# Kernel tuning notes

Hardware: AMD Instinct MI355X
Metric: run time of the kernel (lower is better)

The kernel has to match this reference:

```python
import jax, jax.numpy as jnp
import numpy as np

D_MODEL = 256
NHEAD = 8
NLAYERS = 4
DFF = 1024
PATCH = 8
INPUT = 32
C = 2
DATA_DIM = C * PATCH * PATCH  # 128
P = (INPUT // PATCH) ** 2     # 16
NEG = -1.0e6                  # _neg_large_for_dtype(float32)
EPS = 1e-5


def _ln(x, w, b):
    m = x.mean(-1, keepdims=True)
    v = ((x - m) ** 2).mean(-1, keepdims=True)
    return (x - m) / jnp.sqrt(v + EPS) * w + b


def _forward(img_baseline, acq_dts_float, nan_token, pad_embed, emb_w, emb_b, spatial_pos,
             t_w1, t_b1, t_w2, t_b2, t_w3, t_b3,
             in_proj_w, in_proj_b, out_proj_w, out_proj_b,
             lin1_w, lin1_b, lin2_w, lin2_b, norm1_w, norm1_b, norm2_w, norm2_b,
             mean_w1, mean_b1, mean_w2, mean_b2, lv_w1, lv_b1, lv_w2, lv_b2):
    B, T, Cc, Hh, Ww = img_baseline.shape
    p = PATCH
    gh, gw = Hh // p, Ww // p
    L = T * P
    frame_pad = jnp.all(img_baseline == -9999.0, axis=(2, 3, 4))  # (B,T)
    nan_pix = jnp.isnan(img_baseline)
    token = jnp.clip(nan_token, -10.0, 10.0).reshape(1, 1, Cc, 1, 1)
    x = jnp.clip(jnp.where(nan_pix, token, img_baseline), -10.0, 10.0)

    def patchify(a):  # b t c (h ph)(w pw) -> b t (h w) (c ph pw)
        return a.reshape(B, T, Cc, gh, p, gw, p).transpose(0, 1, 3, 5, 2, 4, 6).reshape(B, T, P, Cc * p * p)

    xp = patchify(x)
    seq_nan = patchify(nan_pix).all(-1).reshape(B, L)
    seq_pad = jnp.broadcast_to(frame_pad[:, :, None], (B, T, P)).reshape(B, L)

    # temporal MLP embedding
    t_in = jnp.where(jnp.isnan(acq_dts_float), 0.0, acq_dts_float)[..., None]  # (B,T,1)
    h = jax.nn.relu(t_in @ t_w1.T + t_b1)
    h = jax.nn.relu(h @ t_w2.T + t_b2)
    temb = h @ t_w3.T + t_b3  # (B,T,D)

    z = xp @ emb_w.T + emb_b + spatial_pos + temb[:, :, None, :]  # (B,T,P,D)
    z = z.reshape(B, L, D_MODEL)
    z = jnp.where(seq_pad[..., None], pad_embed, z)  # masked_scatter of pad_embed

    # additive attention mask: rows with NaN/pad patches are fully masked except diagonal
    masked_rows = seq_nan | seq_pad
    mask = jnp.broadcast_to(jnp.where(masked_rows[:, :, None], NEG, 0.0), (B, L, L))
    eye = jnp.eye(L, dtype=bool)
    mask = jnp.where(eye[None, :, :] & masked_rows[:, :, None], 0.0, mask)
    # key_padding_mask merged additively on key columns
    mask = mask + jnp.where(seq_pad[:, None, :], NEG, 0.0)
    mask = mask[:, None, :, :]  # (B,1,L,L), shared across heads

    dh = D_MODEL // NHEAD
    scale = 1.0 / np.sqrt(dh).astype(np.float32)
    for l in range(NLAYERS):
        qkv = z @ in_proj_w[l].T + in_proj_b[l]
        q, k, v = jnp.split(qkv, 3, axis=-1)
        q = q.reshape(B, L, NHEAD, dh).transpose(0, 2, 1, 3)
        k = k.reshape(B, L, NHEAD, dh).transpose(0, 2, 1, 3)
        v = v.reshape(B, L, NHEAD, dh).transpose(0, 2, 1, 3)
        scores = jnp.einsum('bhqd,bhkd->bhqk', q, k) * scale + mask
        attn = jax.nn.softmax(scores, axis=-1)
        o = jnp.einsum('bhqk,bhkd->bhqd', attn, v).transpose(0, 2, 1, 3).reshape(B, L, D_MODEL)
        o = o @ out_proj_w[l].T + out_proj_b[l]
        z = _ln(z + o, norm1_w[l], norm1_b[l])
        ff = jax.nn.relu(z @ lin1_w[l].T + lin1_b[l]) @ lin2_w[l].T + lin2_b[l]
        z = _ln(z + ff, norm2_w[l], norm2_b[l])

    mean = jnp.clip(jax.nn.relu(z @ mean_w1.T + mean_b1) @ mean_w2.T + mean_b2, -10.0, 10.0)
    logvar = jnp.clip(jax.nn.relu(z @ lv_w1.T + lv_b1) @ lv_w2.T + lv_b2, -10.0, 5.0)

    def unpatch(a):  # b t (h w)(c ph pw) -> b t c (h ph)(w pw)
        return a.reshape(B, T, gh, gw, Cc, p, p).transpose(0, 1, 4, 2, 5, 3, 6).reshape(B, T, Cc, Hh, Ww)

    mean = unpatch(mean.reshape(B, T, P, DATA_DIM))
    logvar = unpatch(logvar.reshape(B, T, P, DATA_DIM))
    return mean[:, -1], logvar[:, -1]


def setup_inputs() -> dict:
    key = jax.random.key(0)
    ks = iter(jax.random.split(key, 48))

    def rn(shape, scale=0.02):
        return jax.random.normal(next(ks), shape, dtype=jnp.float32) * scale

    B, T = 4, 64
    z = lambda s: jnp.zeros(s, jnp.float32)
    return {
        'img_baseline': jax.random.normal(next(ks), (B, T, C, INPUT, INPUT), dtype=jnp.float32),
        'acq_dts_float': jax.random.uniform(next(ks), (B, T), dtype=jnp.float32) * 3000.0,
        'nan_token': rn((C,)),
        'pad_embed': rn((1, 1, D_MODEL)),
        'emb_w': rn((D_MODEL, DATA_DIM)),
        'emb_b': z((D_MODEL,)),
        'spatial_pos': rn((1, 1, P, D_MODEL)),
        't_w1': rn((64, 1)), 't_b1': z((64,)),
        't_w2': rn((128, 64)), 't_b2': z((128,)),
        't_w3': rn((D_MODEL, 128)), 't_b3': z((D_MODEL,)),
        'in_proj_w': rn((NLAYERS, 3 * D_MODEL, D_MODEL)),
        'in_proj_b': z((NLAYERS, 3 * D_MODEL)),
        'out_proj_w': rn((NLAYERS, D_MODEL, D_MODEL)),
        'out_proj_b': z((NLAYERS, D_MODEL)),
        'lin1_w': rn((NLAYERS, DFF, D_MODEL)), 'lin1_b': z((NLAYERS, DFF)),
        'lin2_w': rn((NLAYERS, D_MODEL, DFF)), 'lin2_b': z((NLAYERS, D_MODEL)),
        'norm1_w': jnp.ones((NLAYERS, D_MODEL), jnp.float32), 'norm1_b': z((NLAYERS, D_MODEL)),
        'norm2_w': jnp.ones((NLAYERS, D_MODEL), jnp.float32), 'norm2_b': z((NLAYERS, D_MODEL)),
        'mean_w1': rn((DFF, D_MODEL)), 'mean_b1': z((DFF,)),
        'mean_w2': rn((DATA_DIM, DFF)), 'mean_b2': z((DATA_DIM,)),
        'lv_w1': rn((DFF, D_MODEL)), 'lv_b1': z((DFF,)),
        'lv_w2': rn((DATA_DIM, DFF)), 'lv_b2': z((DATA_DIM,)),
    }


def reference(img_baseline, acq_dts_float, nan_token, pad_embed, emb_w, emb_b, spatial_pos,
              t_w1, t_b1, t_w2, t_b2, t_w3, t_b3,
              in_proj_w, in_proj_b, out_proj_w, out_proj_b,
              lin1_w, lin1_b, lin2_w, lin2_b, norm1_w, norm1_b, norm2_w, norm2_b,
              mean_w1, mean_b1, mean_w2, mean_b2, lv_w1, lv_b1, lv_w2, lv_b2):
    return _forward(img_baseline, acq_dts_float, nan_token, pad_embed, emb_w, emb_b, spatial_pos,
                    t_w1, t_b1, t_w2, t_b2, t_w3, t_b3,
                    in_proj_w, in_proj_b, out_proj_w, out_proj_b,
                    lin1_w, lin1_b, lin2_w, lin2_b, norm1_w, norm1_b, norm2_w, norm2_b,
                    mean_w1, mean_b1, mean_w2, mean_b2, lv_w1, lv_b1, lv_w2, lv_b2)
```

## Files before the change

kernel.cpp:

```cpp
#include <hip/hip_runtime.h>
#include <hip/hip_bf16.h>

#define D_MODEL 256
#define NHEAD 8
#define DH 32
#define NLAYERS 4
#define DFF 1024
#define CC 2
#define DATA_DIM 128
#define PP 16
#define TT 64
#define BB 4
#define LL 1024
#define NEGV -1000000.0f

typedef __bf16 bf16_t;
typedef __bf16 bf16x8 __attribute__((ext_vector_type(8)));
typedef __bf16 bf16x4 __attribute__((ext_vector_type(4)));
typedef float v4f __attribute__((ext_vector_type(4)));

__device__ __forceinline__ bool my_isnan(float v) {
    unsigned u = __float_as_uint(v);
    return (u & 0x7fffffffu) > 0x7f800000u;
}

__device__ __forceinline__ void gld16(bf16_t* l, const bf16_t* g) {
    __builtin_amdgcn_global_load_lds(
        (const __attribute__((address_space(1))) void*)g,
        (__attribute__((address_space(3))) void*)l, 16, 0, 0);
}

__global__ __launch_bounds__(256) void f2b_prep_kernel(
    const float* __restrict__ in_proj_w, bf16_t* __restrict__ inb,
    const float* __restrict__ out_proj_w, bf16_t* __restrict__ outb,
    const float* __restrict__ lin1_w, bf16_t* __restrict__ l1b,
    const float* __restrict__ lin2_w, bf16_t* __restrict__ l2b,
    const float* __restrict__ emb_w, bf16_t* __restrict__ embwb,
    const float* __restrict__ mean_w1, const float* __restrict__ lv_w1, bf16_t* __restrict__ w1b,
    const float* __restrict__ mean_w2, const float* __restrict__ lv_w2, bf16_t* __restrict__ w2b,
    const float* __restrict__ img, const float* __restrict__ acq,
    const float* __restrict__ t_w1, const float* __restrict__ t_b1,
    const float* __restrict__ t_w2, const float* __restrict__ t_b2,
    const float* __restrict__ t_w3, const float* __restrict__ t_b3,
    float* __restrict__ temb, int* __restrict__ framepad) {
    const int n0 = NLAYERS * 768 * D_MODEL;
    const int n1 = NLAYERS * D_MODEL * D_MODEL;
    const int n2 = NLAYERS * DFF * D_MODEL;
    const int n3 = NLAYERS * D_MODEL * DFF;
    const int n4 = D_MODEL * DATA_DIM;
    const int n5 = DFF * D_MODEL;
    const int n6 = DFF * D_MODEL;
    const int n7 = DATA_DIM * DFF;
    const int n8 = DATA_DIM * DFF;
    int tid = threadIdx.x;
    int i = (blockIdx.x * 256 + tid) * 4;
    const float* s = nullptr; bf16_t* d = nullptr;
    if (i < n0) { s = in_proj_w; d = inb; }
    else if ((i -= n0) < n1) { s = out_proj_w; d = outb; }
    else if ((i -= n1) < n2) { s = lin1_w; d = l1b; }
    else if ((i -= n2) < n3) { s = lin2_w; d = l2b; }
    else if ((i -= n3) < n4) { s = emb_w; d = embwb; }
    else if ((i -= n4) < n5) { s = mean_w1; d = w1b; }
    else if ((i -= n5) < n6) { s = lv_w1; d = w1b + n5; }
    else if ((i -= n6) < n7) { s = mean_w2; d = w2b; }
    else if ((i -= n7) < n8) { s = lv_w2; d = w2b + n7; }
    if (s) {
        float4 v = *(const float4*)(s + i);
        bf16x4 o = {(bf16_t)v.x, (bf16_t)v.y, (bf16_t)v.z, (bf16_t)v.w};
        *(bf16x4*)(d + i) = o;
    }

    if (blockIdx.x >= BB * TT) return;
    int f = blockIdx.x;
    __shared__ float h1[64];
    __shared__ float h2[128];
    __shared__ int sAll;
    if (tid == 0) sAll = 1;
    __syncthreads();
    const float* fr = img + (size_t)f * (CC * 32 * 32);
    bool allpad = true;
    #pragma unroll
    for (int k = 0; k < 8; ++k) {
        float v = fr[tid + k * 256];
        allpad = allpad && (v == -9999.0f);
    }
    if (!allpad) sAll = 0;
    __syncthreads();
    if (tid == 0) framepad[f] = sAll;

    float t_in = acq[f];
    if (my_isnan(t_in)) t_in = 0.0f;
    if (tid < 64) h1[tid] = fmaxf(t_w1[tid] * t_in + t_b1[tid], 0.0f);
    __syncthreads();
    if (tid < 128) {
        float a = t_b2[tid];
        #pragma unroll 8
        for (int j = 0; j < 64; ++j) a += t_w2[tid * 64 + j] * h1[j];
        h2[tid] = fmaxf(a, 0.0f);
    }
    __syncthreads();
    {
        float a = t_b3[tid];
        #pragma unroll 8
        for (int j = 0; j < 128; ++j) a += t_w3[tid * 128 + j] * h2[j];
        temb[(size_t)f * D_MODEL + tid] = a;
    }
}

__global__ __launch_bounds__(256) void patchify_kernel(
    const float* __restrict__ img, const float* __restrict__ nan_token,
    const int* __restrict__ framepad,
    bf16_t* __restrict__ xpb, int* __restrict__ masked_rows,
    float* __restrict__ kmaskf) {
    int tid = threadIdx.x;
    int token = blockIdx.x * 2 + (tid >> 7);
    int dd = tid & 127;
    int l = token & 1023, b = token >> 10;
    int t = l >> 4, p = l & 15;
    int c = dd >> 6, pr = (dd >> 3) & 7, pc = dd & 7;
    int hh = (p >> 2) * 8 + pr, ww = (p & 3) * 8 + pc;
    float v = img[(((size_t)(b * TT + t) * CC + c) * 32 + hh) * 32 + ww];
    bool nanp = my_isnan(v);
    if (nanp) v = fminf(fmaxf(nan_token[c], -10.0f), 10.0f);
    v = fminf(fmaxf(v, -10.0f), 10.0f);
    xpb[(size_t)token * DATA_DIM + dd] = (bf16_t)v;

    __shared__ int wAll[4];
    unsigned long long bal = __ballot(nanp);
    if ((tid & 63) == 0) wAll[tid >> 6] = (bal == 0xFFFFFFFFFFFFFFFFull) ? 1 : 0;
    __syncthreads();
    if (tid < 2) {
        int tk = blockIdx.x * 2 + tid;
        int allnan = wAll[tid * 2] & wAll[tid * 2 + 1];
        int fp = framepad[tk >> 4];
        masked_rows[tk] = allnan | fp;
        kmaskf[tk] = fp ? NEGV : 0.0f;
    }
}

__global__ __launch_bounds__(256) void embed_gemm(
    const bf16_t* __restrict__ X, const bf16_t* __restrict__ W,
    const float* __restrict__ emb_b, const float* __restrict__ spatial,
    const float* __restrict__ temb, const float* __restrict__ pad_embed,
    const int* __restrict__ framepad,
    bf16_t* __restrict__ zb) {
    __shared__ __align__(16) bf16_t Xs[2][128 * 64];
    __shared__ __align__(16) bf16_t Ws[2][64 * 64];
    int tid = threadIdx.x;
    int wave = tid >> 6, lane = tid & 63;
    int quad = lane >> 4, l16 = lane & 15;
    int m0 = blockIdx.y * 128, n0 = blockIdx.x * 64;
    const int K = DATA_DIM, N = D_MODEL;

    v4f acc[2][4];
    #pragma unroll
    for (int i = 0; i < 2; ++i)
        #pragma unroll
        for (int j = 0; j < 4; ++j) acc[i][j] = (v4f){0.f, 0.f, 0.f, 0.f};

    int sr = tid >> 3, ss = tid & 7;
    int gc = (ss ^ (sr & 7)) * 8;

#define ESTAGE(bufi, k0)                                                          \
    do {                                                                          \
        _Pragma("unroll")                                                         \
        for (int p = 0; p < 4; ++p) {                                             \
            int r = sr + p * 32;                                                  \
            gld16(Xs[bufi] + r * 64 + ss * 8, X + (size_t)(m0 + r) * K + (k0) + gc); \
        }                                                                         \
        _Pragma("unroll")                                                         \
        for (int p = 0; p < 2; ++p) {                                             \
            int r = sr + p * 32;                                                  \
            gld16(Ws[bufi] + r * 64 + ss * 8, W + (size_t)(n0 + r) * K + (k0) + gc); \
        }                                                                         \
    } while (0)

    ESTAGE(0, 0);
    __syncthreads();
    const int T = K / 64;
    int swl = l16 & 7;
    for (int t = 0; t < T; ++t) {
        int buf = t & 1;
        if (t + 1 < T) ESTAGE(buf ^ 1, (t + 1) * 64);
        const bf16_t* Xc = Xs[buf];
        const bf16_t* Wc = Ws[buf];
        int ra = wave * 32 + l16;
        #pragma unroll
        for (int h = 0; h < 2; ++h) {
            int g8 = ((h * 4 + quad) ^ swl) * 8;
            bf16x8 af0 = *(const bf16x8*)(Xc + ra * 64 + g8);
            bf16x8 af1 = *(const bf16x8*)(Xc + (ra + 16) * 64 + g8);
            #pragma unroll
            for (int nt = 0; nt < 4; ++nt) {
                bf16x8 bfr = *(const bf16x8*)(Wc + (nt * 16 + l16) * 64 + g8);
                acc[0][nt] = __builtin_amdgcn_mfma_f32_16x16x32_bf16(af0, bfr, acc[0][nt], 0, 0, 0);
                acc[1][nt] = __builtin_amdgcn_mfma_f32_16x16x32_bf16(af1, bfr, acc[1][nt], 0, 0, 0);
            }
        }
        __syncthreads();
    }
#undef ESTAGE

    #pragma unroll
    for (int mt = 0; mt < 2; ++mt)
        #pragma unroll
        for (int nt = 0; nt < 4; ++nt) {
            int col = n0 + nt * 16 + l16;
            #pragma unroll
            for (int reg = 0; reg < 4; ++reg) {
                int row = m0 + wave * 32 + mt * 16 + quad * 4 + reg;
                int frame = row >> 4, p = row & 15;
                float v;
                if (framepad[frame]) {
                    v = pad_embed[col];
                } else {
                    v = acc[mt][nt][reg] + emb_b[col] + spatial[p * N + col]
                      + temb[(size_t)frame * N + col];
                }
                zb[(size_t)row * N + col] = (bf16_t)v;
            }
        }
}

template <int MODE, int RELU>
__global__ __launch_bounds__(256) void gemm_mfma(
    const bf16_t* __restrict__ X, const bf16_t* __restrict__ W,
    const float* __restrict__ bias, bf16_t* __restrict__ Y,
    bf16_t* __restrict__ Vt, int M, int N, int K) {
    __shared__ __align__(16) bf16_t Xs[3][128 * 64];
    __shared__ __align__(16) bf16_t Ws[3][64 * 64];
    int tid = threadIdx.x;
    int wave = tid >> 6, lane = tid & 63;
    int quad = lane >> 4, l16 = lane & 15;
    int m0 = blockIdx.y * 128, n0 = blockIdx.x * 64;

    v4f acc[2][4];
    #pragma unroll
    for (int i = 0; i < 2; ++i)
        #pragma unroll
        for (int j = 0; j < 4; ++j) acc[i][j] = (v4f){0.f, 0.f, 0.f, 0.f};

    int sr = tid >> 3, ss = tid & 7;
    int gc = (ss ^ (sr & 7)) * 8;

#define GSTAGE(bufi, k0)                                                          \
    do {                                                                          \
        _Pragma("unroll")                                                         \
        for (int p = 0; p < 4; ++p) {                                             \
            int r = sr + p * 32;                                                  \
            gld16(Xs[bufi] + r * 64 + ss * 8, X + (size_t)(m0 + r) * K + (k0) + gc); \
        }                                                                         \
        _Pragma("unroll")                                                         \
        for (int p = 0; p < 2; ++p) {                                             \
            int r = sr + p * 32;                                                  \
            gld16(Ws[bufi] + r * 64 + ss * 8, W + (size_t)(n0 + r) * K + (k0) + gc); \
        }                                                                         \
    } while (0)

    const int T = K >> 6;
    GSTAGE(0, 0);
    if (T > 1) GSTAGE(1, 64);
    int swl = l16 & 7;
    for (int t = 0; t < T; ++t) {
        int buf = t % 3;
        if (t + 1 < T) asm volatile("s_waitcnt vmcnt(6)" ::: "memory");
        else           asm volatile("s_waitcnt vmcnt(0)" ::: "memory");
        __builtin_amdgcn_s_barrier();
        __builtin_amdgcn_sched_barrier(0);
        if (t + 2 < T) GSTAGE((t + 2) % 3, (t + 2) * 64);
        const bf16_t* Xc = Xs[buf];
        const bf16_t* Wc = Ws[buf];
        int ra = wave * 32 + l16;
        #pragma unroll
        for (int h = 0; h < 2; ++h) {
            int g8 = ((h * 4 + quad) ^ swl) * 8;
            bf16x8 af0 = *(const bf16x8*)(Xc + ra * 64 + g8);
            bf16x8 af1 = *(const bf16x8*)(Xc + (ra + 16) * 64 + g8);
            #pragma unroll
            for (int nt = 0; nt < 4; ++nt) {
                bf16x8 bfr = *(const bf16x8*)(Wc + (nt * 16 + l16) * 64 + g8);
                acc[0][nt] = __builtin_amdgcn_mfma_f32_16x16x32_bf16(af0, bfr, acc[0][nt], 0, 0, 0);
                acc[1][nt] = __builtin_amdgcn_mfma_f32_16x16x32_bf16(af1, bfr, acc[1][nt], 0, 0, 0);
            }
        }
    }
#undef GSTAGE
    __syncthreads();

    if constexpr (MODE == 1) {
        #pragma unroll
        for (int mt = 0; mt < 2; ++mt)
            #pragma unroll
            for (int nt = 0; nt < 4; ++nt) {
                int col = n0 + nt * 16 + l16;
                float bv = bias[col];
                #pragma unroll
                for (int reg = 0; reg < 4; ++reg) {
                    int row = m0 + wave * 32 + mt * 16 + quad * 4 + reg;
                    float v = acc[mt][nt][reg] + bv;
                    if (RELU) v = fmaxf(v, 0.0f);
                    Y[(size_t)row * N + col] = (bf16_t)v;
                }
            }
    } else {
        if (n0 < 512) {
            #pragma unroll
            for (int mt = 0; mt < 2; ++mt)
                #pragma unroll
                for (int nt = 0; nt < 4; ++nt) {
                    int col = n0 + nt * 16 + l16;
                    float bv = bias[col];
                    #pragma unroll
                    for (int reg = 0; reg < 4; ++reg) {
                        int row = m0 + wave * 32 + mt * 16 + quad * 4 + reg;
                        float v = acc[mt][nt][reg] + bv;
                        Y[(size_t)row * 768 + col] = (bf16_t)v;
                    }
                }
        } else {
            bf16_t* VT = &Xs[0][0];
            #pragma unroll
            for (int mt = 0; mt < 2; ++mt)
                #pragma unroll
                for (int nt = 0; nt < 4; ++nt) {
                    int cl = nt * 16 + l16;
                    float bv = bias[n0 + cl];
                    #pragma unroll
                    for (int reg = 0; reg < 4; ++reg) {
                        int rl = wave * 32 + mt * 16 + quad * 4 + reg;
                        VT[cl * 136 + rl] = (bf16_t)(acc[mt][nt][reg] + bv);
                    }
                }
            __syncthreads();
            int b = m0 >> 10, l0m = m0 & 1023;
            int cl = tid >> 2;
            int rbase = (tid & 3) * 8;
            int cg2 = n0 + cl - 512;
            int h = cg2 >> 5, d = cg2 & 31;
            bf16_t* dst = Vt + (((size_t)(b * NHEAD + h)) * DH + d) * LL + l0m;
            #pragma unroll
            for (int u = 0; u < 4; ++u)
                *(uint4*)(dst + rbase + u * 32) = *(const uint4*)(VT + cl * 136 + rbase + u * 32);
        }
    }
}

__global__ __launch_bounds__(256) void gemm_row_ln(
    const bf16_t* __restrict__ X, const bf16_t* __restrict__ W,
    const float* __restrict__ bias, const bf16_t* __restrict__ Zres,
    bf16_t* __restrict__ Y, const float* __restrict__ lnw,
    const float* __restrict__ lnb, int K) {
    __shared__ __align__(16) bf16_t Xs[3][16 * 64];
    __shared__ __align__(16) bf16_t Ws[3][256 * 64];
    int tid = threadIdx.x;
    int wave = tid >> 6, lane = tid & 63;
    int quad = lane >> 4, l16 = lane & 15;
    int mrow0 = blockIdx.x * 16;

    v4f acc[4];
    #pragma unroll
    for (int j = 0; j < 4; ++j) acc[j] = (v4f){0.f, 0.f, 0.f, 0.f};

    int sr = tid >> 3, ss = tid & 7;
    int gc = (ss ^ (sr & 7)) * 8;
    int xl = lane & 31;
    int xrow = wave * 4 + (xl >> 3);
    int xgc = ((xl & 7) ^ (xrow & 7)) * 8;

#define RSTAGE(bufi, k0)                                                          \
    do {                                                                          \
        if (lane < 32)                                                            \
            gld16(Xs[bufi] + wave * 256 + xl * 8,                                 \
                  X + (size_t)(mrow0 + xrow) * K + (k0) + xgc);                   \
        _Pragma("unroll")                                                         \
        for (int p = 0; p < 8; ++p) {                                             \
            int r = sr + p * 32;                                                  \
            gld16(Ws[bufi] + r * 64 + ss * 8, W + (size_t)r * K + (k0) + gc);     \
        }                                                                         \
    } while (0)

    const int T = K >> 6;
    RSTAGE(0, 0);
    RSTAGE(1, 64);
    int swl = l16 & 7;
    for (int t = 0; t < T; ++t) {
        int buf = t % 3;
        if (t + 1 < T) asm volatile("s_waitcnt vmcnt(9)" ::: "memory");
        else           asm volatile("s_waitcnt vmcnt(0)" ::: "memory");
        __builtin_amdgcn_s_barrier();
        __builtin_amdgcn_sched_barrier(0);
        if (t + 2 < T) RSTAGE((t + 2) % 3, (t + 2) * 64);
        const bf16_t* Xc = Xs[buf];
        const bf16_t* Wc = Ws[buf];
        #pragma unroll
        for (int h = 0; h < 2; ++h) {
            int g8 = ((h * 4 + quad) ^ swl) * 8;
            bf16x8 af = *(const bf16x8*)(Xc + l16 * 64 + g8);
            #pragma unroll
            for (int ntl = 0; ntl < 4; ++ntl) {
                int nt = wave * 4 + ntl;
                bf16x8 bfr = *(const bf16x8*)(Wc + (nt * 16 + l16) * 64 + g8);
                acc[ntl] = __builtin_amdgcn_mfma_f32_16x16x32_bf16(af, bfr, acc[ntl], 0, 0, 0);
            }
        }
    }
#undef RSTAGE
    __syncthreads();

    float* psum = (float*)&Xs[0][0];
    float xv[4][4];
    float lw[4], lb[4];
    #pragma unroll
    for (int ntl = 0; ntl < 4; ++ntl) {
        int col = wave * 64 + ntl * 16 + l16;
        float bv = bias[col];
        lw[ntl] = lnw[col];
        lb[ntl] = lnb[col];
        #pragma unroll
        for (int reg = 0; reg < 4; ++reg) {
            int grow = mrow0 + quad * 4 + reg;
            xv[ntl][reg] = acc[ntl][reg] + bv + (float)Zres[(size_t)grow * D_MODEL + col];
        }
    }
    float s[4];
    #pragma unroll
    for (int reg = 0; reg < 4; ++reg) {
        s[reg] = xv[0][reg] + xv[1][reg] + xv[2][reg] + xv[3][reg];
        s[reg] += __shfl_xor(s[reg], 1);
        s[reg] += __shfl_xor(s[reg], 2);
        s[reg] += __shfl_xor(s[reg], 4);
        s[reg] += __shfl_xor(s[reg], 8);
    }
    if (l16 == 0) {
        #pragma unroll
        for (int reg = 0; reg < 4; ++reg)
            psum[wave * 16 + quad * 4 + reg] = s[reg];
    }
    __syncthreads();
    float mean[4];
    #pragma unroll
    for (int reg = 0; reg < 4; ++reg) {
        int row = quad * 4 + reg;
        mean[reg] = (psum[row] + psum[16 + row] + psum[32 + row] + psum[48 + row])
                  * (1.0f / D_MODEL);
    }
    __syncthreads();
    float q[4];
    #pragma unroll
    for (int reg = 0; reg < 4; ++reg) {
        float d0 = xv[0][reg] - mean[reg], d1 = xv[1][reg] - mean[reg];
        float d2 = xv[2][reg] - mean[reg], d3 = xv[3][reg] - mean[reg];
        q[reg] = d0 * d0 + d1 * d1 + d2 * d2 + d3 * d3;
        q[reg] += __shfl_xor(q[reg], 1);
        q[reg] += __shfl_xor(q[reg], 2);
        q[reg] += __shfl_xor(q[reg], 4);
        q[reg] += __shfl_xor(q[reg], 8);
    }
    if (l16 == 0) {
        #pragma unroll
        for (int reg = 0; reg < 4; ++reg)
            psum[wave * 16 + quad * 4 + reg] = q[reg];
    }
    __syncthreads();
    #pragma unroll
    for (int reg = 0; reg < 4; ++reg) {
        int row = quad * 4 + reg;
        float var = (psum[row] + psum[16 + row] + psum[32 + row] + psum[48 + row])
                  * (1.0f / D_MODEL);
        float inv = 1.0f / sqrtf(var + 1e-5f);
        int grow = mrow0 + row;
        #pragma unroll
        for (int ntl = 0; ntl < 4; ++ntl) {
            int col = wave * 64 + ntl * 16 + l16;
            Y[(size_t)grow * D_MODEL + col] =
                (bf16_t)((xv[ntl][reg] - mean[reg]) * inv * lw[ntl] + lb[ntl]);
        }
    }
}

__global__ __launch_bounds__(256) void attn_mfma(
    const bf16_t* __restrict__ qkvb, const bf16_t* __restrict__ Vt,
    const int* __restrict__ masked_rows, const float* __restrict__ kmaskf,
    bf16_t* __restrict__ Ob) {
    __shared__ __align__(16) bf16_t Ks[2][128 * 40];
    __shared__ __align__(16) bf16_t Vs[2][32 * 136];
    __shared__ __align__(16) float  Kms[2][128];
    __shared__ __align__(16) bf16_t Ps[4][16 * 136];

    int tid = threadIdx.x;
    int wave = tid >> 6, lane = tid & 63;
    int quad = lane >> 4, l16 = lane & 15;
    int bid = blockIdx.x;
    int h = bid & 7, b = (bid >> 3) & 3, qt = bid >> 5;
    int q0 = qt * 64 + wave * 16;
    const float scale = 0.17677669529663687f;

    bf16x8 qf = *(const bf16x8*)(qkvb + ((size_t)(b * LL) + q0 + l16) * 768 + h * DH + quad * 8);

    int mq = masked_rows[b * LL + q0 + l16];
    int qg = q0 + l16;

    float lrun = 0.0f;
    v4f oacc[2];
    oacc[0] = (v4f){0.f, 0.f, 0.f, 0.f};
    oacc[1] = (v4f){0.f, 0.f, 0.f, 0.f};

    int kr = tid >> 1, kh = (tid & 1) * 16;
    int vd = tid >> 3, vs0 = (tid & 7) * 8;
    const bf16_t* Kbase = qkvb + (size_t)(b * LL) * 768 + 256 + h * DH;
    const bf16_t* Vbase = Vt + (((size_t)(b * NHEAD + h)) * DH) * LL;
    const float* kmbase = kmaskf + b * LL;

    uint4 ka, kb, va, vb;
    float kmg;
    #define LOADC(c)                                                            \
        do {                                                                    \
            int _k0 = (c) * 128;                                                \
            ka = *(const uint4*)(Kbase + (size_t)(_k0 + kr) * 768 + kh);        \
            kb = *(const uint4*)(Kbase + (size_t)(_k0 + kr) * 768 + kh + 8);    \
            va = *(const uint4*)(Vbase + (size_t)vd * LL + _k0 + vs0);          \
            vb = *(const uint4*)(Vbase + (size_t)vd * LL + _k0 + 64 + vs0);     \
            kmg = (tid < 128) ? kmbase[_k0 + tid] : 0.0f;                       \
        } while (0)
    #define WRITEBUF(buf)                                                       \
        do {                                                                    \
            *(uint4*)(Ks[(buf)] + kr * 40 + kh) = ka;                           \
            *(uint4*)(Ks[(buf)] + kr * 40 + kh + 8) = kb;                       \
            *(uint4*)(Vs[(buf)] + vd * 136 + vs0) = va;                         \
            *(uint4*)(Vs[(buf)] + vd * 136 + 64 + vs0) = vb;                    \
            if (tid < 128) Kms[(buf)][tid] = kmg;                               \
        } while (0)

    LOADC(0);
    WRITEBUF(0);
    LOADC(1);

    bf16_t* Pw = Ps[wave];
    for (int c = 0; c < 8; ++c) {
        __syncthreads();
        int cur = c & 1;
        if (c + 1 < 8) WRITEBUF(cur ^ 1);
        if (c + 2 < 8) LOADC(c + 2);

        int k0 = c * 128;
        const bf16_t* Kc = Ks[cur];
        const bf16_t* Vc = Vs[cur];
        const float* kmc = Kms[cur];

        v4f sf[8];
        #pragma unroll
        for (int nt = 0; nt < 8; ++nt) {
            bf16x8 kf = *(const bf16x8*)(Kc + (nt * 16 + l16) * 40 + quad * 8);
            v4f zf = (v4f){0.f, 0.f, 0.f, 0.f};
            sf[nt] = __builtin_amdgcn_mfma_f32_16x16x32_bf16(kf, qf, zf, 0, 0, 0);
        }

        #pragma unroll
        for (int nt = 0; nt < 8; ++nt) {
            int kbase_nt = k0 + nt * 16 + quad * 4;
            float4 kmv = *(const float4*)(kmc + nt * 16 + quad * 4);
            float pv[4];
            #pragma unroll
            for (int reg = 0; reg < 4; ++reg) {
                float km = (reg == 0) ? kmv.x : (reg == 1) ? kmv.y : (reg == 2) ? kmv.z : kmv.w;
                float v = sf[nt][reg] * scale + km;
                if (mq && (qg != kbase_nt + reg)) v += NEGV;
                float p = __expf(v);
                lrun += p;
                pv[reg] = p;
            }
            bf16x4 pp = {(bf16_t)pv[0], (bf16_t)pv[1], (bf16_t)pv[2], (bf16_t)pv[3]};
            *(bf16x4*)(Pw + l16 * 136 + nt * 16 + quad * 4) = pp;
        }

        #pragma unroll
        for (int kt = 0; kt < 4; ++kt) {
            bf16x8 pf = *(const bf16x8*)(Pw + l16 * 136 + kt * 32 + quad * 8);
            #pragma unroll
            for (int nt2 = 0; nt2 < 2; ++nt2) {
                bf16x8 vf = *(const bf16x8*)(Vc + (nt2 * 16 + l16) * 136 + kt * 32 + quad * 8);
                oacc[nt2] = __builtin_amdgcn_mfma_f32_16x16x32_bf16(pf, vf, oacc[nt2], 0, 0, 0);
            }
        }
    }
    #undef LOADC
    #undef WRITEBUF

    lrun += __shfl_xor(lrun, 16);
    lrun += __shfl_xor(lrun, 32);
    float lq[4];
    #pragma unroll
    for (int reg = 0; reg < 4; ++reg) lq[reg] = __shfl(lrun, quad * 4 + reg);

    #pragma unroll
    for (int nt2 = 0; nt2 < 2; ++nt2)
        #pragma unroll
        for (int reg = 0; reg < 4; ++reg) {
            size_t row = (size_t)(b * LL) + q0 + quad * 4 + reg;
            Ob[row * 256 + h * DH + nt2 * 16 + l16] = (bf16_t)(oacc[nt2][reg] / lq[reg]);
        }
}

__global__ __launch_bounds__(256) void head_h_kernel(
    const bf16_t* __restrict__ zb, const bf16_t* __restrict__ W1b,
    const float* __restrict__ mean_b1, const float* __restrict__ lv_b1,
    bf16_t* __restrict__ hb) {
    __shared__ __align__(16) bf16_t Xs[2][64 * 32 * 2];
    __shared__ __align__(16) bf16_t Ws[2][64 * 32 * 2];
    int tid = threadIdx.x;
    int wave = tid >> 6, lane = tid & 63;
    int quad = lane >> 4, l16 = lane & 15;
    int head = blockIdx.y;
    int n0 = blockIdx.x * 64;
    const bf16_t* W1h = W1b + (size_t)head * DFF * D_MODEL;
    const float* B1f = head ? lv_b1 : mean_b1;
    bf16_t* hbh = hb + (size_t)head * 64 * DFF;

    v4f acc[4];
    #pragma unroll
    for (int j = 0; j < 4; ++j) acc[j] = (v4f){0.f, 0.f, 0.f, 0.f};

    int sr = tid >> 3, ss = tid & 7;
    int gc = (ss ^ (sr & 7)) * 8;

#define HSTAGE(bufi, k0)                                                          \
    do {                                                                          \
        _Pragma("unroll")                                                         \
        for (int p = 0; p < 2; ++p) {                                             \
            int r = sr + p * 32;                                                  \
            const bf16_t* xr = zb + (size_t)((r >> 4) * LL + (TT - 1) * PP + (r & 15)) * D_MODEL; \
            gld16(Xs[bufi] + r * 64 + ss * 8, xr + (k0) + gc);                    \
            gld16(Ws[bufi] + r * 64 + ss * 8, W1h + (size_t)(n0 + r) * D_MODEL + (k0) + gc); \
        }                                                                         \
    } while (0)

    HSTAGE(0, 0);
    __syncthreads();
    const int T = D_MODEL / 64;
    int swl = l16 & 7;
    for (int t = 0; t < T; ++t) {
        int buf = t & 1;
        if (t + 1 < T) HSTAGE(buf ^ 1, (t + 1) * 64);
        const bf16_t* Xc = Xs[buf];
        const bf16_t* Wc = Ws[buf];
        int ra = wave * 16 + l16;
        #pragma unroll
        for (int h = 0; h < 2; ++h) {
            int g8 = ((h * 4 + quad) ^ swl) * 8;
            bf16x8 af = *(const bf16x8*)(Xc + ra * 64 + g8);
            #pragma unroll
            for (int nt = 0; nt < 4; ++nt) {
                bf16x8 bfr = *(const bf16x8*)(Wc + (nt * 16 + l16) * 64 + g8);
                acc[nt] = __builtin_amdgcn_mfma_f32_16x16x32_bf16(af, bfr, acc[nt], 0, 0, 0);
            }
        }
        __syncthreads();
    }
#undef HSTAGE

    #pragma unroll
    for (int nt = 0; nt < 4; ++nt) {
        int col = n0 + nt * 16 + l16;
        float bv = B1f[col];
        #pragma unroll
        for (int reg = 0; reg < 4; ++reg) {
            int row = wave * 16 + quad * 4 + reg;
            hbh[(size_t)row * DFF + col] = (bf16_t)fmaxf(acc[nt][reg] + bv, 0.0f);
        }
    }
}

__global__ __launch_bounds__(256) void head_out_kernel(
    const bf16_t* __restrict__ hb, const bf16_t* __restrict__ W2b,
    const float* __restrict__ mean_b2, const float* __restrict__ lv_b2,
    float* __restrict__ out) {
    __shared__ __align__(16) bf16_t hrow[DFF];
    int tid = threadIdx.x;
    int bid = blockIdx.x;
    int head = bid >> 7, rr = (bid >> 1) & 63, half = bid & 1;
    int b = rr >> 4, p = rr & 15;

    if (tid < 128)
        *(uint4*)(hrow + tid * 8) =
            *(const uint4*)(hb + ((size_t)head * 64 + rr) * DFF + tid * 8);
    __syncthreads();

    int ol = tid >> 2, quarter = tid & 3;
    int o = half * 64 + ol;
    const bf16_t* wrow = W2b + ((size_t)head * DATA_DIM + o) * DFF + quarter * 256;
    const bf16_t* hseg = hrow + quarter * 256;
    float acc = 0.0f;
    #pragma unroll 8
    for (int j = 0; j < 32; ++j) {
        bf16x8 w = *(const bf16x8*)(wrow + j * 8);
        bf16x8 hv = *(const bf16x8*)(hseg + j * 8);
        #pragma unroll
        for (int e = 0; e < 8; ++e) acc += (float)w[e] * (float)hv[e];
    }
    acc += __shfl_xor(acc, 1);
    acc += __shfl_xor(acc, 2);
    if (quarter == 0) {
        const float* B2 = head ? lv_b2 : mean_b2;
        float hi = head ? 5.0f : 10.0f;
        float v = fminf(fmaxf(acc + B2[o], -10.0f), hi);
        int c = o >> 6;
        int pr = (o >> 3) & 7, pc = o & 7;
        int hh = (p >> 2) * 8 + pr, ww = (p & 3) * 8 + pc;
        out[(size_t)head * 8192 + ((size_t)(b * CC + c)) * 1024 + hh * 32 + ww] = v;
    }
}

extern "C" void kernel_launch(void* const* d_in, const int* in_sizes, int n_in,
                              void* d_out, int out_size, void* d_ws, size_t ws_size,
                              hipStream_t stream) {
    const float* img        = (const float*)d_in[0];
    const float* acq        = (const float*)d_in[1];
    const float* nan_token  = (const float*)d_in[2];
    const float* pad_embed  = (const float*)d_in[3];
    const float* emb_w      = (const float*)d_in[4];
    const float* emb_b      = (const float*)d_in[5];
    const float* spatial    = (const float*)d_in[6];
    const float* t_w1       = (const float*)d_in[7];
    const float* t_b1       = (const float*)d_in[8];
    const float* t_w2       = (const float*)d_in[9];
    const float* t_b2       = (const float*)d_in[10];
    const float* t_w3       = (const float*)d_in[11];
    const float* t_b3       = (const float*)d_in[12];
    const float* in_proj_w  = (const float*)d_in[13];
    const float* in_proj_b  = (const float*)d_in[14];
    const float* out_proj_w = (const float*)d_in[15];
    const float* out_proj_b = (const float*)d_in[16];
    const float* lin1_w     = (const float*)d_in[17];
    const float* lin1_b     = (const float*)d_in[18];
    const float* lin2_w     = (const float*)d_in[19];
    const float* lin2_b     = (const float*)d_in[20];
    const float* norm1_w    = (const float*)d_in[21];
    const float* norm1_b    = (const float*)d_in[22];
    const float* norm2_w    = (const float*)d_in[23];
    const float* norm2_b    = (const float*)d_in[24];
    const float* mean_w1    = (const float*)d_in[25];
    const float* mean_b1    = (const float*)d_in[26];
    const float* mean_w2    = (const float*)d_in[27];
    const float* mean_b2    = (const float*)d_in[28];
    const float* lv_w1      = (const float*)d_in[29];
    const float* lv_b1      = (const float*)d_in[30];
    const float* lv_w2      = (const float*)d_in[31];
    const float* lv_b2      = (const float*)d_in[32];

    const int M = BB * LL;

    char* wsb = (char*)d_ws;
    float* temb    = (float*)wsb;                    wsb += (size_t)BB * TT * D_MODEL * 4;
    float* kmaskf  = (float*)wsb;                    wsb += M * 4;
    int* framepad  = (int*)wsb;                      wsb += BB * TT * 4;
    int* masked    = (int*)wsb;                      wsb += M * 4;
    wsb = (char*)(((uintptr_t)wsb + 255) & ~(uintptr_t)255);
    bf16_t* zb     = (bf16_t*)wsb;                   wsb += (size_t)M * D_MODEL * 2;
    bf16_t* xpb    = (bf16_t*)wsb;                   wsb += (size_t)M * DATA_DIM * 2;
    bf16_t* qkvb   = (bf16_t*)wsb;                   wsb += (size_t)M * 768 * 2;
    bf16_t* VtG    = (bf16_t*)wsb;                   wsb += (size_t)M * D_MODEL * 2;
    bf16_t* attnb  = (bf16_t*)wsb;                   wsb += (size_t)M * D_MODEL * 2;
    bf16_t* ff1b   = (bf16_t*)wsb;                   wsb += (size_t)M * DFF * 2;
    bf16_t* inb    = (bf16_t*)wsb;                   wsb += (size_t)NLAYERS * 768 * D_MODEL * 2;
    bf16_t* outb   = (bf16_t*)wsb;                   wsb += (size_t)NLAYERS * D_MODEL * D_MODEL * 2;
    bf16_t* l1b    = (bf16_t*)wsb;                   wsb += (size_t)NLAYERS * DFF * D_MODEL * 2;
    bf16_t* l2b    = (bf16_t*)wsb;                   wsb += (size_t)NLAYERS * D_MODEL * DFF * 2;
    bf16_t* embwb  = (bf16_t*)wsb;                   wsb += (size_t)D_MODEL * DATA_DIM * 2;
    bf16_t* w1b    = (bf16_t*)wsb;                   wsb += (size_t)2 * DFF * D_MODEL * 2;
    bf16_t* w2b    = (bf16_t*)wsb;                   wsb += (size_t)2 * DATA_DIM * DFF * 2;
    bf16_t* hb     = (bf16_t*)wsb;                   wsb += (size_t)2 * 64 * DFF * 2;

    float* outF = (float*)d_out;

    {
        int tot = NLAYERS * 768 * D_MODEL + NLAYERS * D_MODEL * D_MODEL +
                  NLAYERS * DFF * D_MODEL + NLAYERS * D_MODEL * DFF +
                  D_MODEL * DATA_DIM + 2 * DFF * D_MODEL + 2 * DATA_DIM * DFF;
        f2b_prep_kernel<<<(tot / 4 + 255) / 256, 256, 0, stream>>>(
            in_proj_w, inb, out_proj_w, outb, lin1_w, l1b, lin2_w, l2b,
            emb_w, embwb, mean_w1, lv_w1, w1b, mean_w2, lv_w2, w2b,
            img, acq, t_w1, t_b1, t_w2, t_b2, t_w3, t_b3, temb, framepad);
    }

    patchify_kernel<<<M / 2, 256, 0, stream>>>(img, nan_token, framepad, xpb, masked, kmaskf);
    embed_gemm<<<dim3(D_MODEL / 64, M / 128), 256, 0, stream>>>(
        xpb, embwb, emb_b, spatial, temb, pad_embed, framepad, zb);

    for (int l = 0; l < NLAYERS; ++l) {
        gemm_mfma<2, 0><<<dim3(768 / 64, M / 128), 256, 0, stream>>>(
            zb, inb + (size_t)l * 768 * D_MODEL, in_proj_b + (size_t)l * 768,
            qkvb, VtG, M, 768, D_MODEL);
        attn_mfma<<<BB * NHEAD * (LL / 64), 256, 0, stream>>>(qkvb, VtG, masked, kmaskf, attnb);
        gemm_row_ln<<<M / 16, 256, 0, stream>>>(
            attnb, outb + (size_t)l * D_MODEL * D_MODEL, out_proj_b + (size_t)l * D_MODEL,
            zb, zb, norm1_w + l * D_MODEL, norm1_b + l * D_MODEL, D_MODEL);
        gemm_mfma<1, 1><<<dim3(DFF / 64, M / 128), 256, 0, stream>>>(
            zb, l1b + (size_t)l * DFF * D_MODEL, lin1_b + (size_t)l * DFF,
            ff1b, nullptr, M, DFF, D_MODEL);
        gemm_row_ln<<<M / 16, 256, 0, stream>>>(
            ff1b, l2b + (size_t)l * D_MODEL * DFF, lin2_b + (size_t)l * D_MODEL,
            zb, zb, norm2_w + l * D_MODEL, norm2_b + l * D_MODEL, DFF);
    }

    head_h_kernel<<<dim3(DFF / 64, 2), 256, 0, stream>>>(zb, w1b, mean_b1, lv_b1, hb);
    head_out_kernel<<<256, 256, 0, stream>>>(hb, w2b, mean_b2, lv_b2, outF);
}
```

Baseline: 389.8 us.

## Fuse out-proj+LayerNorm with FF1 GEMM+ReLU in one row-block kernel

```diff
diff --git a/kernel.cpp b/kernel.cpp
--- a/kernel.cpp
+++ b/kernel.cpp
@@ -478,6 +478,204 @@
     }
 }
 
+__global__ __launch_bounds__(256) void gemm_row_ln_ff(
+    const bf16_t* __restrict__ X, const bf16_t* __restrict__ W,
+    const float* __restrict__ bias, const bf16_t* __restrict__ Zres,
+    bf16_t* __restrict__ Y, const float* __restrict__ lnw,
+    const float* __restrict__ lnb,
+    const bf16_t* __restrict__ W1, const float* __restrict__ b1,
+    bf16_t* __restrict__ H) {
+    __shared__ __align__(16) bf16_t Xs[3][16 * 64];
+    __shared__ __align__(16) bf16_t Ynorm[16 * 256];
+    __shared__ __align__(16) bf16_t Ws[3][256 * 64];
+    int tid = threadIdx.x;
+    int wave = tid >> 6, lane = tid & 63;
+    int quad = lane >> 4, l16 = lane & 15;
+    int mrow0 = blockIdx.x * 16;
+    const int K = D_MODEL;
+
+    v4f acc[4];
+    #pragma unroll
+    for (int j = 0; j < 4; ++j) acc[j] = (v4f){0.f, 0.f, 0.f, 0.f};
+
+    int sr = tid >> 3, ss = tid & 7;
+    int gc = (ss ^ (sr & 7)) * 8;
+    int xl = lane & 31;
+    int xrow = wave * 4 + (xl >> 3);
+    int xgc = ((xl & 7) ^ (xrow & 7)) * 8;
+    int swl = l16 & 7;
+
+#define ASTAGE(bufi, k0)                                                          \
+    do {                                                                          \
+        if (lane < 32)                                                            \
+            gld16(Xs[bufi] + wave * 256 + xl * 8,                                 \
+                  X + (size_t)(mrow0 + xrow) * K + (k0) + xgc);                   \
+        _Pragma("unroll")                                                         \
+        for (int p = 0; p < 8; ++p) {                                             \
+            int r = sr + p * 32;                                                  \
+            gld16(Ws[bufi] + r * 64 + ss * 8, W + (size_t)r * K + (k0) + gc);     \
+        }                                                                         \
+    } while (0)
+
+    const int TA = K >> 6;
+    ASTAGE(0, 0);
+    ASTAGE(1, 64);
+    for (int t = 0; t < TA; ++t) {
+        int buf = t % 3;
+        if (t + 1 < TA) asm volatile("s_waitcnt vmcnt(9)" ::: "memory");
+        else            asm volatile("s_waitcnt vmcnt(0)" ::: "memory");
+        __builtin_amdgcn_s_barrier();
+        __builtin_amdgcn_sched_barrier(0);
+        if (t + 2 < TA) ASTAGE((t + 2) % 3, (t + 2) * 64);
+        const bf16_t* Xc = Xs[buf];
+        const bf16_t* Wc = Ws[buf];
+        #pragma unroll
+        for (int h = 0; h < 2; ++h) {
+            int g8 = ((h * 4 + quad) ^ swl) * 8;
+            bf16x8 af = *(const bf16x8*)(Xc + l16 * 64 + g8);
+            #pragma unroll
+            for (int ntl = 0; ntl < 4; ++ntl) {
+                int nt = wave * 4 + ntl;
+                bf16x8 bfr = *(const bf16x8*)(Wc + (nt * 16 + l16) * 64 + g8);
+                acc[ntl] = __builtin_amdgcn_mfma_f32_16x16x32_bf16(af, bfr, acc[ntl], 0, 0, 0);
+            }
+        }
+    }
+#undef ASTAGE
+    __syncthreads();
+
+#define BSTAGE(bufi, s)                                                           \
+    do {                                                                          \
+        int _pn = (s) >> 2, _ks = (s) & 3;                                        \
+        _Pragma("unroll")                                                         \
+        for (int p = 0; p < 8; ++p) {                                             \
+            int r = sr + p * 32;                                                  \
+            gld16(Ws[bufi] + r * 64 + ss * 8,                                     \
+                  W1 + (size_t)(_pn * 256 + r) * 256 + _ks * 64 + gc);            \
+        }                                                                         \
+    } while (0)
+
+    BSTAGE(0, 0);
+    BSTAGE(1, 1);
+
+    float* psum = (float*)&Xs[0][0];
+    float xv[4][4];
+    float lw[4], lb[4];
+    #pragma unroll
+    for (int ntl = 0; ntl < 4; ++ntl) {
+        int col = wave * 64 + ntl * 16 + l16;
+        float bv = bias[col];
+        lw[ntl] = lnw[col];
+        lb[ntl] = lnb[col];
+        #pragma unroll
+        for (int reg = 0; reg < 4; ++reg) {
+            int grow = mrow0 + quad * 4 + reg;
+            xv[ntl][reg] = acc[ntl][reg] + bv + (float)Zres[(size_t)grow * D_MODEL + col];
+        }
+    }
+    float s1[4];
+    #pragma unroll
+    for (int reg = 0; reg < 4; ++reg) {
+        s1[reg] = xv[0][reg] + xv[1][reg] + xv[2][reg] + xv[3][reg];
+        s1[reg] += __shfl_xor(s1[reg], 1);
+        s1[reg] += __shfl_xor(s1[reg], 2);
+        s1[reg] += __shfl_xor(s1[reg], 4);
+        s1[reg] += __shfl_xor(s1[reg], 8);
+    }
+    if (l16 == 0) {
+        #pragma unroll
+        for (int reg = 0; reg < 4; ++reg)
+            psum[wave * 16 + quad * 4 + reg] = s1[reg];
+    }
+    __syncthreads();
+    float mean[4];
+    #pragma unroll
+    for (int reg = 0; reg < 4; ++reg) {
+        int row = quad * 4 + reg;
+        mean[reg] = (psum[row] + psum[16 + row] + psum[32 + row] + psum[48 + row])
+                  * (1.0f / D_MODEL);
+    }
+    __syncthreads();
+    float q[4];
+    #pragma unroll
+    for (int reg = 0; reg < 4; ++reg) {
+        float d0 = xv[0][reg] - mean[reg], d1 = xv[1][reg] - mean[reg];
+        float d2 = xv[2][reg] - mean[reg], d3 = xv[3][reg] - mean[reg];
+        q[reg] = d0 * d0 + d1 * d1 + d2 * d2 + d3 * d3;
+        q[reg] += __shfl_xor(q[reg], 1);
+        q[reg] += __shfl_xor(q[reg], 2);
+        q[reg] += __shfl_xor(q[reg], 4);
+        q[reg] += __shfl_xor(q[reg], 8);
+    }
+    if (l16 == 0) {
+        #pragma unroll
+        for (int reg = 0; reg < 4; ++reg)
+            psum[wave * 16 + quad * 4 + reg] = q[reg];
+    }
+    __syncthreads();
+    #pragma unroll
+    for (int reg = 0; reg < 4; ++reg) {
+        int row = quad * 4 + reg;
+        float var = (psum[row] + psum[16 + row] + psum[32 + row] + psum[48 + row])
+                  * (1.0f / D_MODEL);
+        float inv = 1.0f / sqrtf(var + 1e-5f);
+        int grow = mrow0 + row;
+        #pragma unroll
+        for (int ntl = 0; ntl < 4; ++ntl) {
+            int col = wave * 64 + ntl * 16 + l16;
+            float nv = (xv[ntl][reg] - mean[reg]) * inv * lw[ntl] + lb[ntl];
+            bf16_t nb = (bf16_t)nv;
+            Y[(size_t)grow * D_MODEL + col] = nb;
+            int within = ntl * 16 + l16;
+            int g = within >> 3;
+            int slot = g ^ (row & 7);
+            Ynorm[row * 256 + wave * 64 + slot * 8 + (within & 7)] = nb;
+        }
+    }
+    __syncthreads();
+
+    v4f accB[4];
+    #pragma unroll
+    for (int j = 0; j < 4; ++j) accB[j] = (v4f){0.f, 0.f, 0.f, 0.f};
+
+    for (int s = 0; s < 16; ++s) {
+        int buf = s % 3;
+        if (s + 1 < 16) asm volatile("s_waitcnt vmcnt(8)" ::: "memory");
+        else            asm volatile("s_waitcnt vmcnt(0)" ::: "memory");
+        __builtin_amdgcn_s_barrier();
+        __builtin_amdgcn_sched_barrier(0);
+        if (s + 2 < 16) BSTAGE((s + 2) % 3, s + 2);
+        int ks = s & 3;
+        const bf16_t* Wc = Ws[buf];
+        #pragma unroll
+        for (int h = 0; h < 2; ++h) {
+            int g8 = ((h * 4 + quad) ^ swl) * 8;
+            bf16x8 af = *(const bf16x8*)(Ynorm + l16 * 256 + ks * 64 + g8);
+            #pragma unroll
+            for (int ntl = 0; ntl < 4; ++ntl) {
+                bf16x8 bfr = *(const bf16x8*)(Wc + (wave * 64 + ntl * 16 + l16) * 64 + g8);
+                accB[ntl] = __builtin_amdgcn_mfma_f32_16x16x32_bf16(af, bfr, accB[ntl], 0, 0, 0);
+            }
+        }
+        if (ks == 3) {
+            int pn = s >> 2;
+            #pragma unroll
+            for (int ntl = 0; ntl < 4; ++ntl) {
+                int gcol = pn * 256 + wave * 64 + ntl * 16 + l16;
+                float bv = b1[gcol];
+                #pragma unroll
+                for (int reg = 0; reg < 4; ++reg) {
+                    int grow = mrow0 + quad * 4 + reg;
+                    H[(size_t)grow * DFF + gcol] =
+                        (bf16_t)fmaxf(accB[ntl][reg] + bv, 0.0f);
+                }
+                accB[ntl] = (v4f){0.f, 0.f, 0.f, 0.f};
+            }
+        }
+    }
+#undef BSTAGE
+}
+
 __global__ __launch_bounds__(256) void attn_mfma(
     const bf16_t* __restrict__ qkvb, const bf16_t* __restrict__ Vt,
     const int* __restrict__ masked_rows, const float* __restrict__ kmaskf,
@@ -791,12 +989,10 @@
             zb, inb + (size_t)l * 768 * D_MODEL, in_proj_b + (size_t)l * 768,
             qkvb, VtG, M, 768, D_MODEL);
         attn_mfma<<<BB * NHEAD * (LL / 64), 256, 0, stream>>>(qkvb, VtG, masked, kmaskf, attnb);
-        gemm_row_ln<<<M / 16, 256, 0, stream>>>(
+        gemm_row_ln_ff<<<M / 16, 256, 0, stream>>>(
             attnb, outb + (size_t)l * D_MODEL * D_MODEL, out_proj_b + (size_t)l * D_MODEL,
-            zb, zb, norm1_w + l * D_MODEL, norm1_b + l * D_MODEL, D_MODEL);
-        gemm_mfma<1, 1><<<dim3(DFF / 64, M / 128), 256, 0, stream>>>(
-            zb, l1b + (size_t)l * DFF * D_MODEL, lin1_b + (size_t)l * DFF,
-            ff1b, nullptr, M, DFF, D_MODEL);
+            zb, zb, norm1_w + l * D_MODEL, norm1_b + l * D_MODEL,
+            l1b + (size_t)l * DFF * D_MODEL, lin1_b + (size_t)l * DFF, ff1b);
         gemm_row_ln<<<M / 16, 256, 0, stream>>>(
             ff1b, l2b + (size_t)l * D_MODEL * DFF, lin2_b + (size_t)l * D_MODEL,
             zb, zb, norm2_w + l * D_MODEL, norm2_b + l * D_MODEL, DFF);
```

After: 414.1 us. +6.2%, slower.
